# Kernel tuning notes

Hardware: AMD Instinct MI355X
Metric: run time of the kernel (lower is better)

## Reference

```python
import jax, jax.numpy as jnp
import numpy as np

IN_F = 4096
OUT_F = 4096
GROUP = 64  # quant group size along axis=0 of the reshaped weight


def setup_inputs() -> dict:
    key = jax.random.key(0)
    k1, k2, k3, k4, k5 = jax.random.split(key, 5)
    n_groups = IN_F * OUT_F // GROUP  # 262144
    x = jax.random.normal(k1, (8, 512, IN_F), dtype=jnp.float32)
    # packed 4-bit codes: two codes per byte, split along axis 0 (pack_4bit_u8)
    W_q = jax.random.randint(k2, (GROUP // 2, n_groups), 0, 256, dtype=jnp.int32)
    # scale here is meta['scale'] = 1/raw_scale (the dequant multiplier)
    scale = jax.random.uniform(k3, (1, n_groups), dtype=jnp.float32, minval=1e-3, maxval=1e-2)
    zero = jax.random.uniform(k4, (1, n_groups), dtype=jnp.float32, minval=0.0, maxval=15.0)
    bias = jax.random.normal(k5, (OUT_F,), dtype=jnp.float32) * 0.01
    return {"x": x, "W_q": W_q, "scale": scale, "zero": zero, "bias": bias}


def _dequantize(W_q, scale, zero):
    # unpack_4bit_u8: cat([(p >> 4) & 0xF, p & 0xF], axis=0) -> [GROUP, n_groups]
    hi = (W_q >> 4) & 0xF
    lo = W_q & 0xF
    W_q_p = jnp.concatenate([hi, lo], axis=0).astype(jnp.float32)
    # (W_q - zero) * scale, then reshape back to [out_features, in_features]
    return ((W_q_p - zero) * scale).reshape(OUT_F, IN_F)


def reference(x, W_q, scale, zero, bias):
    W_est = _dequantize(W_q, scale, zero)  # [OUT_F, IN_F]
    out = jnp.einsum('bsi,oi->bso', x, W_est)  # x @ W.T
    return out + bias
```

## Files before the change

### kernel.cpp

```cpp
#include <hip/hip_runtime.h>
#include <hip/hip_bf16.h>
#include <stdint.h>


#define IN_F  4096
#define OUT_F 4096
#define MROWS 4096

#define BM 256
#define BN 256
#define BK 64
#define NT (IN_F / BK)

typedef __attribute__((ext_vector_type(8))) __bf16 bf16x8;
typedef __attribute__((ext_vector_type(4))) float f32x4;

__device__ __forceinline__ ushort f2bf(float f) {
    uint32_t u = __float_as_uint(f);
    u += 0x7fffu + ((u >> 16) & 1u);
    return (ushort)(u >> 16);
}

__global__ void conv_x(const float* __restrict__ x, ushort* __restrict__ xb, int n) {
    int i = (blockIdx.x * blockDim.x + threadIdx.x) * 4;
    if (i >= n) return;
    float4 v = *(const float4*)(x + i);
    *(ushort4*)(xb + i) = make_ushort4(f2bf(v.x), f2bf(v.y), f2bf(v.z), f2bf(v.w));
}

__global__ void dequant(const int* __restrict__ Wq, const float* __restrict__ scale,
                        const float* __restrict__ zero, ushort* __restrict__ West) {
    int t = blockIdx.x * blockDim.x + threadIdx.x;
    int flat = t << 2;
    int p = flat >> 18;
    int c = flat & 262143;
    int j = c >> 12;
    int i = c & 4095;

    int4 q = *(const int4*)(Wq + flat);
    float4 sc = *(const float4*)(scale + c);
    float4 zr = *(const float4*)(zero + c);

    int   qv[4] = {q.x, q.y, q.z, q.w};
    float sv[4] = {sc.x, sc.y, sc.z, sc.w};
    float zv[4] = {zr.x, zr.y, zr.z, zr.w};

    ushort hi[4], lo[4];
#pragma unroll
    for (int e = 0; e < 4; ++e) {
        hi[e] = f2bf(((float)((qv[e] >> 4) & 0xF) - zv[e]) * sv[e]);
        lo[e] = f2bf(((float)(qv[e] & 0xF) - zv[e]) * sv[e]);
    }
    size_t o_hi = (size_t)(p * 64 + j) * IN_F + i;
    size_t o_lo = (size_t)((p + 32) * 64 + j) * IN_F + i;
    *(ushort4*)(West + o_hi) = make_ushort4(hi[0], hi[1], hi[2], hi[3]);
    *(ushort4*)(West + o_lo) = make_ushort4(lo[0], lo[1], lo[2], lo[3]);
}

__device__ __forceinline__ void gload16(const ushort* g, const ushort* l) {
    __builtin_amdgcn_global_load_lds((const __attribute__((address_space(1))) void*)g,
                                     (__attribute__((address_space(3))) void*)l,
                                     16, 0, 0);
}


#define VMCNT4 asm volatile("s_waitcnt vmcnt(4)" ::: "memory");
#define VMCNT0 asm volatile("s_waitcnt vmcnt(0)" ::: "memory");
#define BAR    __builtin_amdgcn_s_barrier();

#define DS_A(kk, mh)                                                               \
    _Pragma("unroll") for (int mf = 0; mf < 4; ++mf)                               \
        afr[mf] = *(const bf16x8*)&lds[(size_t)b * 32768 + (kk) * 8192 +           \
            ((wr * 128 + (mh) * 64 + mf * 16 + rl) * 4 + hx) * 8];

#define DS_B(kk)                                                                   \
    _Pragma("unroll") for (int nf = 0; nf < 4; ++nf)                               \
        bfr[nf] = *(const bf16x8*)&lds[(size_t)b * 32768 + 16384 + (kk) * 8192 +   \
            ((wc * 64 + nf * 16 + rl) * 4 + hx) * 8];

#define MFMA16(mh)                                                                 \
    __builtin_amdgcn_s_setprio(1);                                                 \
    _Pragma("unroll") for (int mf = 0; mf < 4; ++mf)                               \
    _Pragma("unroll") for (int nf = 0; nf < 4; ++nf)                               \
        acc[(mh) * 4 + mf][nf] = __builtin_amdgcn_mfma_f32_16x16x32_bf16(          \
            afr[mf], bfr[nf], acc[(mh) * 4 + mf][nf], 0, 0, 0);                    \
    __builtin_amdgcn_s_setprio(0);

__global__ __launch_bounds__(512, 2) void gemm_bt(const ushort* __restrict__ A,
                                                  const ushort* __restrict__ B,
                                                  const float* __restrict__ bias,
                                                  float* __restrict__ C) {
    __shared__ alignas(16) ushort lds[65536];

    const int tid  = threadIdx.x;
    const int wave = tid >> 6;
    const int lane = tid & 63;
    const int rl   = lane & 15;
    const int hh   = lane >> 4;
    const int hx   = hh ^ ((rl >> 1) & 3);

    int bid = blockIdx.x;
    int swz = (bid & 7) * 32 + (bid >> 3);
    const int m0 = (swz >> 4) * BM;
    const int n0 = (swz & 15) * BN;
    const int wr = wave >> 2;
    const int wc = wave & 3;

    f32x4 acc[8][4];
    f32x4 z4 = {0.f, 0.f, 0.f, 0.f};
#pragma unroll
    for (int i = 0; i < 8; ++i)
#pragma unroll
        for (int j = 0; j < 4; ++j) acc[i][j] = z4;

    auto stageA = [&](int nb, int kh, int kcol) {
#pragma unroll
        for (int q = 0; q < 2; ++q) {
            int cu = q * 512 + wave * 64;
            int s  = cu + lane;
            int r  = s >> 2;
            int h  = (s & 3) ^ ((r >> 1) & 3);
            gload16(A + (size_t)(m0 + r) * IN_F + kcol + h * 8,
                    &lds[(size_t)nb * 32768 + kh * 8192 + cu * 8]);
        }
    };
    auto stageB = [&](int nb, int kh, int kcol) {
#pragma unroll
        for (int q = 0; q < 2; ++q) {
            int cu = q * 512 + wave * 64;
            int s  = cu + lane;
            int r  = s >> 2;
            int h  = (s & 3) ^ ((r >> 1) & 3);
            gload16(B + (size_t)(n0 + r) * IN_F + kcol + h * 8,
                    &lds[(size_t)nb * 32768 + 16384 + kh * 8192 + cu * 8]);
        }
    };

    stageA(0, 0, 0);
    stageB(0, 0, 0);
    stageA(0, 1, 32);
    stageB(0, 1, 32);
    VMCNT4;
    BAR;

    for (int T = 0; T < NT; ++T) {
        const int b  = T & 1;
        const int nb = b ^ 1;
        const int kn = ((T + 1) & (NT - 1)) * BK;
        bf16x8 afr[4], bfr[4];

        DS_B(0) DS_A(0, 0)
        stageA(nb, 0, kn);
        BAR; MFMA16(0) BAR;

        DS_A(0, 1)
        stageB(nb, 0, kn);
        VMCNT4;
        BAR; MFMA16(1) BAR;

        DS_B(1) DS_A(1, 0)
        stageA(nb, 1, kn + 32);
        BAR; MFMA16(0) BAR;

        DS_A(1, 1)
        stageB(nb, 1, kn + 32);
        VMCNT4;
        BAR; MFMA16(1) BAR;
    }
    VMCNT0;

#pragma unroll
    for (int nf = 0; nf < 4; ++nf) {
        int col = n0 + wc * 64 + nf * 16 + rl;
        float bv = bias[col];
#pragma unroll
        for (int mfa = 0; mfa < 8; ++mfa) {
            int rbase = m0 + wr * 128 + mfa * 16 + (hh << 2);
#pragma unroll
            for (int v = 0; v < 4; ++v)
                C[(size_t)(rbase + v) * OUT_F + col] = acc[mfa][nf][v] + bv;
        }
    }
}

extern "C" void kernel_launch(void* const* d_in, const int* in_sizes, int n_in,
                              void* d_out, int out_size, void* d_ws, size_t ws_size,
                              hipStream_t stream) {
    const float* x     = (const float*)d_in[0];
    const int*   Wq    = (const int*)d_in[1];
    const float* scale = (const float*)d_in[2];
    const float* zero  = (const float*)d_in[3];
    const float* bias  = (const float*)d_in[4];
    float* out = (float*)d_out;

    ushort* xb   = (ushort*)d_ws;
    ushort* West = (ushort*)d_ws + (size_t)MROWS * IN_F;

    conv_x<<<(MROWS * IN_F / 4 + 255) / 256, 256, 0, stream>>>(x, xb, MROWS * IN_F);
    dequant<<<(32 * 262144 / 4 + 255) / 256, 256, 0, stream>>>(Wq, scale, zero, West);

    gemm_bt<<<(MROWS / BM) * (OUT_F / BN), 512, 0, stream>>>(xb, West, bias, out);
}
```

Baseline: 272.1 us.

## Merge prep kernels and deepen GEMM global-to-LDS prefetch by one stage

Merges the x-to-bf16 conversion and the weight dequantization into one prep kernel that branches on block index, which removes one launch and the gap between two small kernels. In the GEMM main loop the global-to-LDS load schedule is shifted so the next-next A k-half is issued one phase earlier, and the wait count is raised from 4 to 6. This keeps more loads in flight per wave, so memory latency is hidden better behind the MFMA phases. The cost is tighter reasoning about reuse of LDS buffers and wait counts.

```diff
diff --git a/kernel.cpp b/kernel.cpp
--- a/kernel.cpp
+++ b/kernel.cpp
@@ -21,40 +21,44 @@
     return (ushort)(u >> 16);
 }
 
-__global__ void conv_x(const float* __restrict__ x, ushort* __restrict__ xb, int n) {
-    int i = (blockIdx.x * blockDim.x + threadIdx.x) * 4;
-    if (i >= n) return;
-    float4 v = *(const float4*)(x + i);
-    *(ushort4*)(xb + i) = make_ushort4(f2bf(v.x), f2bf(v.y), f2bf(v.z), f2bf(v.w));
-}
-
-__global__ void dequant(const int* __restrict__ Wq, const float* __restrict__ scale,
-                        const float* __restrict__ zero, ushort* __restrict__ West) {
-    int t = blockIdx.x * blockDim.x + threadIdx.x;
-    int flat = t << 2;
-    int p = flat >> 18;
-    int c = flat & 262143;
-    int j = c >> 12;
-    int i = c & 4095;
-
-    int4 q = *(const int4*)(Wq + flat);
-    float4 sc = *(const float4*)(scale + c);
-    float4 zr = *(const float4*)(zero + c);
-
-    int   qv[4] = {q.x, q.y, q.z, q.w};
-    float sv[4] = {sc.x, sc.y, sc.z, sc.w};
-    float zv[4] = {zr.x, zr.y, zr.z, zr.w};
-
-    ushort hi[4], lo[4];
-#pragma unroll
-    for (int e = 0; e < 4; ++e) {
-        hi[e] = f2bf(((float)((qv[e] >> 4) & 0xF) - zv[e]) * sv[e]);
-        lo[e] = f2bf(((float)(qv[e] & 0xF) - zv[e]) * sv[e]);
+#define CONV_BLK (MROWS * IN_F / 4 / 256)
+#define DQ_BLK   (32 * 262144 / 4 / 256)
+
+__global__ void prep(const float* __restrict__ x, ushort* __restrict__ xb,
+                     const int* __restrict__ Wq, const float* __restrict__ scale,
+                     const float* __restrict__ zero, ushort* __restrict__ West) {
+    int blk = blockIdx.x;
+    if (blk < CONV_BLK) {
+        int i = (blk * 256 + threadIdx.x) * 4;
+        float4 v = *(const float4*)(x + i);
+        *(ushort4*)(xb + i) = make_ushort4(f2bf(v.x), f2bf(v.y), f2bf(v.z), f2bf(v.w));
+    } else {
+        int t = (blk - CONV_BLK) * 256 + threadIdx.x;
+        int flat = t << 2;
+        int p = flat >> 18;
+        int c = flat & 262143;
+        int j = c >> 12;
+        int i = c & 4095;
+
+        int4 q = *(const int4*)(Wq + flat);
+        float4 sc = *(const float4*)(scale + c);
+        float4 zr = *(const float4*)(zero + c);
+
+        int   qv[4] = {q.x, q.y, q.z, q.w};
+        float sv[4] = {sc.x, sc.y, sc.z, sc.w};
+        float zv[4] = {zr.x, zr.y, zr.z, zr.w};
+
+        ushort hi[4], lo[4];
+#pragma unroll
+        for (int e = 0; e < 4; ++e) {
+            hi[e] = f2bf(((float)((qv[e] >> 4) & 0xF) - zv[e]) * sv[e]);
+            lo[e] = f2bf(((float)(qv[e] & 0xF) - zv[e]) * sv[e]);
+        }
+        size_t o_hi = (size_t)(p * 64 + j) * IN_F + i;
+        size_t o_lo = (size_t)((p + 32) * 64 + j) * IN_F + i;
+        *(ushort4*)(West + o_hi) = make_ushort4(hi[0], hi[1], hi[2], hi[3]);
+        *(ushort4*)(West + o_lo) = make_ushort4(lo[0], lo[1], lo[2], lo[3]);
     }
-    size_t o_hi = (size_t)(p * 64 + j) * IN_F + i;
-    size_t o_lo = (size_t)((p + 32) * 64 + j) * IN_F + i;
-    *(ushort4*)(West + o_hi) = make_ushort4(hi[0], hi[1], hi[2], hi[3]);
-    *(ushort4*)(West + o_lo) = make_ushort4(lo[0], lo[1], lo[2], lo[3]);
 }
 
 __device__ __forceinline__ void gload16(const ushort* g, const ushort* l) {
@@ -64,7 +68,7 @@
 }
 
 
-#define VMCNT4 asm volatile("s_waitcnt vmcnt(4)" ::: "memory");
+#define VMCNT6 asm volatile("s_waitcnt vmcnt(6)" ::: "memory");
 #define VMCNT0 asm volatile("s_waitcnt vmcnt(0)" ::: "memory");
 #define BAR    __builtin_amdgcn_s_barrier();
 
@@ -140,31 +144,33 @@
     stageB(0, 0, 0);
     stageA(0, 1, 32);
     stageB(0, 1, 32);
-    VMCNT4;
+    stageA(1, 0, BK);
+    VMCNT6;
     BAR;
 
     for (int T = 0; T < NT; ++T) {
-        const int b  = T & 1;
-        const int nb = b ^ 1;
-        const int kn = ((T + 1) & (NT - 1)) * BK;
+        const int b   = T & 1;
+        const int nb  = b ^ 1;
+        const int kn1 = ((T + 1) & (NT - 1)) * BK;
+        const int kn2 = ((T + 2) & (NT - 1)) * BK;
         bf16x8 afr[4], bfr[4];
 
         DS_B(0) DS_A(0, 0)
-        stageA(nb, 0, kn);
+        stageB(nb, 0, kn1);
         BAR; MFMA16(0) BAR;
 
         DS_A(0, 1)
-        stageB(nb, 0, kn);
-        VMCNT4;
+        stageA(nb, 1, kn1 + 32);
+        VMCNT6;
         BAR; MFMA16(1) BAR;
 
         DS_B(1) DS_A(1, 0)
-        stageA(nb, 1, kn + 32);
+        stageB(nb, 1, kn1 + 32);
         BAR; MFMA16(0) BAR;
 
         DS_A(1, 1)
-        stageB(nb, 1, kn + 32);
-        VMCNT4;
+        stageA(b, 0, kn2);
+        VMCNT6;
         BAR; MFMA16(1) BAR;
     }
     VMCNT0;
@@ -196,8 +202,6 @@
     ushort* xb   = (ushort*)d_ws;
     ushort* West = (ushort*)d_ws + (size_t)MROWS * IN_F;
 
-    conv_x<<<(MROWS * IN_F / 4 + 255) / 256, 256, 0, stream>>>(x, xb, MROWS * IN_F);
-    dequant<<<(32 * 262144 / 4 + 255) / 256, 256, 0, stream>>>(Wq, scale, zero, West);
-
+    prep<<<CONV_BLK + DQ_BLK, 256, 0, stream>>>(x, xb, Wq, scale, zero, West);
     gemm_bt<<<(MROWS / BM) * (OUT_F / BN), 512, 0, stream>>>(xb, West, bias, out);
 }
```

New measurement: 268.4 us. Within noise of the previous version (-1.4%).
